# Kernel tuning notes

Hardware: AMD Instinct MI355X
Metric: run time of the kernel (lower is better)

## Reference

```python
import jax, jax.numpy as jnp
import numpy as np

D_IN, D_K, D_V = 512, 256, 256
B, S = 8, 2048

def _glorot(key, shape):
    fan_in, fan_out = shape[0], shape[-1]
    lim = np.sqrt(6.0 / (fan_in + fan_out))
    return jax.random.uniform(key, shape, jnp.float32, -lim, lim)

def setup_inputs() -> dict:
    key = jax.random.key(0)
    ks = jax.random.split(key, 9)
    return {
        "q_in": jax.random.normal(ks[0], (B, S, D_IN), jnp.float32),
        "k_in": jax.random.normal(ks[1], (B, S, D_IN), jnp.float32),
        "v_in": jax.random.normal(ks[2], (B, S, D_IN), jnp.float32),
        "Wq": _glorot(ks[3], (D_IN, D_K)),
        "bq": _glorot(ks[4], (1, D_K))[0],
        "Wk": _glorot(ks[5], (D_IN, D_K)),
        "bk": _glorot(ks[6], (1, D_K))[0],
        "Wv": _glorot(ks[7], (D_IN, D_V)),
        "bv": _glorot(ks[8], (1, D_V))[0],
    }

def reference(q_in, k_in, v_in, Wq, bq, Wk, bk, Wv, bv):
    # Dense projections (with bias, glorot-init'ed bias as in the original)
    q = q_in @ Wq + bq            # [B, S, d_k]
    k = k_in @ Wk + bk            # [B, S, d_k]
    v = v_in @ Wv + bv            # [B, S, d_v]
    scale = 1.0 / np.sqrt(D_K).astype(np.float32)
    # full attention matrix, scaled (map_fn in original == elementwise divide)
    attn = jnp.einsum('bqd,bkd->bqk', q, k) * scale  # [B, S, S]
    attn = jax.nn.softmax(attn, axis=-1)
    return jnp.einsum('bqk,bkd->bqd', attn, v)       # [B, S, d_v]
```

## Files before the change

### kernel.cpp

```cpp
#include <hip/hip_runtime.h>
#include <hip/hip_bf16.h>


typedef __attribute__((ext_vector_type(4))) float f32x4;
typedef __attribute__((ext_vector_type(8))) short s16x8;
typedef __attribute__((ext_vector_type(4))) short s16x4;
typedef unsigned int u32;

static __device__ __forceinline__ short f2bf(float x) {
  __hip_bfloat16 h = __float2bfloat16(x);
  return *reinterpret_cast<short*>(&h);
}
static __device__ __forceinline__ u32 pack2bf(float lo, float hi) {
  return (u32)(unsigned short)f2bf(lo) | ((u32)(unsigned short)f2bf(hi) << 16);
}
static __device__ __forceinline__ void gload16(const void* g, void* l) {
  __builtin_amdgcn_global_load_lds(
      (const __attribute__((address_space(1))) u32*)g,
      (__attribute__((address_space(3))) u32*)l, 16, 0, 0);
}

__global__ __launch_bounds__(256) void proj3(
    const float* __restrict__ q_in, const float* __restrict__ k_in,
    const float* __restrict__ v_in, const float* __restrict__ bq,
    const float* __restrict__ bk, const float* __restrict__ bv,
    const float* __restrict__ Wq, const float* __restrict__ Wk,
    const float* __restrict__ Wv, short* __restrict__ qs,
    char* __restrict__ ks, char* __restrict__ vt) {
  const int flat = blockIdx.x;
  const int ord = (flat & 7) * 96 + (flat >> 3);
  const int z = ord >> 8;
  const int rem = ord & 255;
  const int n0 = (rem & 1) * 128;
  const int m0 = (rem >> 1) * 128;
  const float* X = z == 0 ? q_in : z == 1 ? k_in : v_in;
  const float* W = z == 0 ? Wq : z == 1 ? Wk : Wv;
  const float* bias = z == 0 ? bq : z == 1 ? bk : bv;
  const float sc = z == 0 ? 0.0625f : 1.0f;

  __shared__ short As[128][40];
  __shared__ short Bs[128][40];

  const int tid = threadIdx.x;
  const int lane = tid & 63;
  const int wid = tid >> 6;
  const int wr = wid >> 1, wc = wid & 1;
  const int g = lane >> 4, c = lane & 15;

  f32x4 acc[4][4];
#pragma unroll
  for (int m = 0; m < 4; m++)
#pragma unroll
    for (int n = 0; n < 4; n++) acc[m][n] = (f32x4)0.0f;

  const int arow = tid >> 1, ahalf = tid & 1;
  const int bn = tid & 127, bhalf = tid >> 7;

  for (int kt = 0; kt < 16; ++kt) {
    const int k0 = kt * 32;
    const float* ap = &X[(m0 + arow) * 512 + k0 + ahalf * 16];
    f32x4 a0 = *(const f32x4*)(ap + 0);
    f32x4 a1 = *(const f32x4*)(ap + 4);
    f32x4 a2 = *(const f32x4*)(ap + 8);
    f32x4 a3 = *(const f32x4*)(ap + 12);
    float wv[16];
#pragma unroll
    for (int j = 0; j < 16; j++)
      wv[j] = W[(k0 + bhalf * 16 + j) * 256 + n0 + bn] * sc;
    __syncthreads();
    s16x8 ac0, ac1, w0, w1;
#pragma unroll
    for (int i = 0; i < 4; i++) {
      ac0[i] = f2bf(a0[i]);
      ac0[i + 4] = f2bf(a1[i]);
      ac1[i] = f2bf(a2[i]);
      ac1[i + 4] = f2bf(a3[i]);
    }
#pragma unroll
    for (int j = 0; j < 8; j++) {
      w0[j] = f2bf(wv[j]);
      w1[j] = f2bf(wv[8 + j]);
    }
    *(s16x8*)&As[arow][ahalf * 16 + 0] = ac0;
    *(s16x8*)&As[arow][ahalf * 16 + 8] = ac1;
    *(s16x8*)&Bs[bn][bhalf * 16 + 0] = w0;
    *(s16x8*)&Bs[bn][bhalf * 16 + 8] = w1;
    __syncthreads();
    s16x8 af[4], bfr[4];
#pragma unroll
    for (int m = 0; m < 4; m++)
      af[m] = *(const s16x8*)&As[wr * 64 + m * 16 + c][g * 8];
#pragma unroll
    for (int n = 0; n < 4; n++)
      bfr[n] = *(const s16x8*)&Bs[wc * 64 + n * 16 + c][g * 8];
#pragma unroll
    for (int m = 0; m < 4; m++)
#pragma unroll
      for (int n = 0; n < 4; n++)
        acc[m][n] = __builtin_amdgcn_mfma_f32_16x16x32_bf16(af[m], bfr[n],
                                                            acc[m][n], 0, 0, 0);
  }

  float bv4[4];
#pragma unroll
  for (int n = 0; n < 4; n++) bv4[n] = bias[n0 + wc * 64 + n * 16 + c] * sc;

  if (z == 0) {
#pragma unroll
    for (int m = 0; m < 4; m++) {
      const int row0 = m0 + wr * 64 + m * 16 + g * 4;
#pragma unroll
      for (int n = 0; n < 4; n++) {
        const int col = n0 + wc * 64 + n * 16 + c;
#pragma unroll
        for (int r = 0; r < 4; r++)
          qs[(row0 + r) * 512 + col] = f2bf(acc[m][n][r] + bv4[n]);
      }
    }
  } else if (z == 1) {
#pragma unroll
    for (int m = 0; m < 4; m++) {
      const int row0 = m0 + wr * 64 + m * 16 + g * 4;
#pragma unroll
      for (int n = 0; n < 4; n++) {
        const int col = n0 + wc * 64 + n * 16 + c;
#pragma unroll
        for (int r = 0; r < 4; r++) {
          const int rowg = row0 + r;
          const int bb = rowg >> 11, s = rowg & 2047;
          const int tt = s >> 5, rr = s & 31;
          const u32 off = (u32)(rr * 512 + col * 2) ^ ((u32)(rr & 7) << 4);
          *(short*)(ks + ((size_t)(bb * 64 + tt) << 14) + off) =
              f2bf(acc[m][n][r] + bv4[n]);
        }
      }
    }
  } else {
#pragma unroll
    for (int m = 0; m < 4; m++) {
      const int row0 = m0 + wr * 64 + m * 16 + g * 4;
      const int bb = row0 >> 11, s = row0 & 2047;
      const int tt = s >> 5, kvl = s & 31;
#pragma unroll
      for (int n = 0; n < 4; n++) {
        const int col = n0 + wc * 64 + n * 16 + c;
        s16x4 pk;
#pragma unroll
        for (int r = 0; r < 4; r++) pk[r] = f2bf(acc[m][n][r] + bv4[n]);
        const u32 off = (u32)(col * 64 + kvl * 2) ^ ((u32)(col & 7) << 4);
        *(s16x4*)(vt + ((size_t)(bb * 64 + tt) << 14) + off) = pk;
      }
    }
  }
}

__global__ __launch_bounds__(512, 1) void attn_fused(
    const short* __restrict__ qs, const char* __restrict__ ksb,
    const char* __restrict__ vtb, float* __restrict__ out) {
  const int bid = blockIdx.x;
  const int b = bid & 7;
  const int q0 = (bid >> 3) * 64;

  __shared__ __align__(16) char smem[141312];

  const int tid = threadIdx.x;
  const int lane = tid & 63;
  const int wid = tid >> 6;
  const int grp = wid >> 2;
  const int wq = wid & 3;
  const int gtid = tid & 255;
  const int g = lane >> 4, c = lane & 15;

  const char* ktiles = ksb + ((size_t)b << 20);
  const char* vtiles = vtb + ((size_t)b << 20);

  char* gbase = smem + grp * 65536;
  short* Ps = (short*)(smem + 131072 + wid * 1280);

  s16x8 qf[8];
  {
    const int qrow = (b << 11) + q0 + wq * 16 + c;
#pragma unroll
    for (int d = 0; d < 8; d++)
      qf[d] = *(const s16x8*)&qs[qrow * 512 + d * 32 + g * 8];
  }

  f32x4 o[16];
#pragma unroll
  for (int f = 0; f < 16; f++) o[f] = (f32x4)0.0f;
  float m_l = -1e30f;
  float l_l = 0.f;

  const u32 xr = (u32)(c & 7) << 4;

  auto STAGE = [&](int t, int sel) {
    const size_t toff = (size_t)(grp * 32 + t) << 14;
    char* kd = gbase + sel * 32768;
    char* vd = kd + 16384;
    const char* ksrc = ktiles + toff + gtid * 16;
    const char* vsrc = vtiles + toff + gtid * 16;
#pragma unroll
    for (int i = 0; i < 4; i++) {
      gload16(ksrc + i * 4096, kd + gtid * 16 + i * 4096);
      gload16(vsrc + i * 4096, vd + gtid * 16 + i * 4096);
    }
  };

  STAGE(0, 0);
  __syncthreads();

  for (int t = 0; t < 32; ++t) {
    const int sel = t & 1;
    if (t < 31) STAGE(t + 1, sel ^ 1);

    const char* Kb = gbase + sel * 32768;
    const char* Vb = Kb + 16384;

    f32x4 sf[2];
    sf[0] = (f32x4)0.0f;
    sf[1] = (f32x4)0.0f;
    __builtin_amdgcn_s_setprio(1);
#pragma unroll
    for (int d = 0; d < 8; ++d) {
      const u32 k0off = ((u32)(c * 512 + d * 64 + g * 16)) ^ xr;
      const s16x8 kf0 = *(const s16x8*)(Kb + k0off);
      const s16x8 kf1 = *(const s16x8*)(Kb + (k0off + 8192));
      sf[0] = __builtin_amdgcn_mfma_f32_16x16x32_bf16(kf0, qf[d], sf[0], 0, 0, 0);
      sf[1] = __builtin_amdgcn_mfma_f32_16x16x32_bf16(kf1, qf[d], sf[1], 0, 0, 0);
    }
    __builtin_amdgcn_s_setprio(0);

    float mx = sf[0][0];
#pragma unroll
    for (int nf = 0; nf < 2; nf++)
#pragma unroll
      for (int r = 0; r < 4; r++) mx = fmaxf(mx, sf[nf][r]);
    mx = fmaxf(mx, __shfl_xor(mx, 16, 64));
    mx = fmaxf(mx, __shfl_xor(mx, 32, 64));
    if (__any(mx > m_l + 8.f)) {
      const float mn = fmaxf(m_l, mx);
      const float scr = __expf(m_l - mn);
      m_l = mn;
      l_l *= scr;
      float so[4];
#pragma unroll
      for (int r = 0; r < 4; r++) so[r] = __shfl(scr, g * 4 + r, 64);
#pragma unroll
      for (int f = 0; f < 16; f++)
#pragma unroll
        for (int r = 0; r < 4; r++) o[f][r] *= so[r];
    }
    float sum = 0.f;
#pragma unroll
    for (int nf = 0; nf < 2; nf++)
#pragma unroll
      for (int r = 0; r < 4; r++) {
        const float p = __expf(sf[nf][r] - m_l);
        sf[nf][r] = p;
        sum += p;
      }
    sum += __shfl_xor(sum, 16, 64);
    sum += __shfl_xor(sum, 32, 64);
    l_l += sum;

#pragma unroll
    for (int nf = 0; nf < 2; nf++) {
      const int base = c * 40 + nf * 16 + g * 4;
      *(u32*)&Ps[base] = pack2bf(sf[nf][0], sf[nf][1]);
      *(u32*)&Ps[base + 2] = pack2bf(sf[nf][2], sf[nf][3]);
    }

    const s16x8 pa = *(const s16x8*)&Ps[c * 40 + g * 8];
    __builtin_amdgcn_s_setprio(1);
#pragma unroll
    for (int f = 0; f < 16; ++f) {
      const u32 voff = ((u32)((f * 16 + c) * 64 + g * 16)) ^ xr;
      const s16x8 vf = *(const s16x8*)(Vb + voff);
      o[f] = __builtin_amdgcn_mfma_f32_16x16x32_bf16(pa, vf, o[f], 0, 0, 0);
    }
    __builtin_amdgcn_s_setprio(0);

    __syncthreads();
  }

  float(*Om)[260] = (float(*)[260])smem;
  float(*Ml)[2] = (float(*)[2])(smem + 66560);
  float m0r[4], l0r[4];
#pragma unroll
  for (int r = 0; r < 4; r++) {
    m0r[r] = __shfl(m_l, g * 4 + r, 64);
    l0r[r] = __shfl(l_l, g * 4 + r, 64);
  }
  if (grp == 1) {
#pragma unroll
    for (int f = 0; f < 16; f++)
#pragma unroll
      for (int r = 0; r < 4; r++)
        Om[wq * 16 + g * 4 + r][f * 16 + c] = o[f][r];
    if (g == 0) {
      Ml[wq * 16 + c][0] = m_l;
      Ml[wq * 16 + c][1] = l_l;
    }
  }
  __syncthreads();
  if (grp == 0) {
    float e0v[4], e1v[4], inv[4];
#pragma unroll
    for (int r = 0; r < 4; r++) {
      const int rw = wq * 16 + g * 4 + r;
      const float m1 = Ml[rw][0], l1 = Ml[rw][1];
      const float ms = fmaxf(m0r[r], m1);
      e0v[r] = __expf(m0r[r] - ms);
      e1v[r] = __expf(m1 - ms);
      inv[r] = 1.0f / (l0r[r] * e0v[r] + l1 * e1v[r]);
    }
#pragma unroll
    for (int f = 0; f < 16; f++) {
#pragma unroll
      for (int r = 0; r < 4; r++) {
        const int rw = wq * 16 + g * 4 + r;
        out[((b << 11) + q0 + rw) * 256 + f * 16 + c] =
            (o[f][r] * e0v[r] + Om[rw][f * 16 + c] * e1v[r]) * inv[r];
      }
    }
  }
}

extern "C" void kernel_launch(void* const* d_in, const int* in_sizes, int n_in,
                              void* d_out, int out_size, void* d_ws,
                              size_t ws_size, hipStream_t stream) {
  const float* q_in = (const float*)d_in[0];
  const float* k_in = (const float*)d_in[1];
  const float* v_in = (const float*)d_in[2];
  const float* Wq = (const float*)d_in[3];
  const float* bq = (const float*)d_in[4];
  const float* Wk = (const float*)d_in[5];
  const float* bk = (const float*)d_in[6];
  const float* Wv = (const float*)d_in[7];
  const float* bv = (const float*)d_in[8];
  float* out = (float*)d_out;

  char* ws = (char*)d_ws;
  short* qsb = (short*)d_out;
  char* ksb = ws;
  char* vtb = ws + (8 << 20);

  proj3<<<dim3(768), dim3(256), 0, stream>>>(q_in, k_in, v_in, bq, bk, bv, Wq,
                                             Wk, Wv, qsb, ksb, vtb);
  attn_fused<<<dim3(256), dim3(512), 0, stream>>>(qsb, ksb, vtb, out);
}
```

Measured before the change: 105.0 us.

## Split attention KV range across four wave groups and retile projection GEMM

The attention kernel moves from 512 to 1024 threads, so four wave groups each handle a quarter of the KV sequence (16 tiles each). The per-group K/V staging is single-buffered with two barriers per iteration in place of double-buffered prefetch, and the four partial softmax states are merged through shared memory. The projection kernel switches to 64x256 tiles with full-width N, which re-reads each input row once instead of twice. The intent is to spread the serial KV loop over more waves; the cost is lost load/compute overlap and a serialized four-step reduction.

```diff
diff --git a/kernel.cpp b/kernel.cpp
--- a/kernel.cpp
+++ b/kernel.cpp
@@ -27,19 +27,16 @@
     const float* __restrict__ Wq, const float* __restrict__ Wk,
     const float* __restrict__ Wv, short* __restrict__ qs,
     char* __restrict__ ks, char* __restrict__ vt) {
-  const int flat = blockIdx.x;
-  const int ord = (flat & 7) * 96 + (flat >> 3);
-  const int z = ord >> 8;
-  const int rem = ord & 255;
-  const int n0 = (rem & 1) * 128;
-  const int m0 = (rem >> 1) * 128;
+  const int bid = blockIdx.x;
+  const int z = bid % 3;
+  const int m0 = (bid / 3) * 64;
   const float* X = z == 0 ? q_in : z == 1 ? k_in : v_in;
   const float* W = z == 0 ? Wq : z == 1 ? Wk : Wv;
   const float* bias = z == 0 ? bq : z == 1 ? bk : bv;
   const float sc = z == 0 ? 0.0625f : 1.0f;
 
-  __shared__ short As[128][40];
-  __shared__ short Bs[128][40];
+  __shared__ short As[64][40];
+  __shared__ short Bs[256][40];
 
   const int tid = threadIdx.x;
   const int lane = tid & 63;
@@ -47,83 +44,77 @@
   const int wr = wid >> 1, wc = wid & 1;
   const int g = lane >> 4, c = lane & 15;
 
-  f32x4 acc[4][4];
-#pragma unroll
-  for (int m = 0; m < 4; m++)
-#pragma unroll
-    for (int n = 0; n < 4; n++) acc[m][n] = (f32x4)0.0f;
-
-  const int arow = tid >> 1, ahalf = tid & 1;
-  const int bn = tid & 127, bhalf = tid >> 7;
+  f32x4 acc[2][8];
+#pragma unroll
+  for (int m = 0; m < 2; m++)
+#pragma unroll
+    for (int n = 0; n < 8; n++) acc[m][n] = (f32x4)0.0f;
+
+  const int arow = tid >> 2, aseg = tid & 3;
+  const int bn = tid;
 
   for (int kt = 0; kt < 16; ++kt) {
     const int k0 = kt * 32;
-    const float* ap = &X[(m0 + arow) * 512 + k0 + ahalf * 16];
+    const float* ap = &X[(m0 + arow) * 512 + k0 + aseg * 8];
     f32x4 a0 = *(const f32x4*)(ap + 0);
     f32x4 a1 = *(const f32x4*)(ap + 4);
-    f32x4 a2 = *(const f32x4*)(ap + 8);
-    f32x4 a3 = *(const f32x4*)(ap + 12);
-    float wv[16];
-#pragma unroll
-    for (int j = 0; j < 16; j++)
-      wv[j] = W[(k0 + bhalf * 16 + j) * 256 + n0 + bn] * sc;
-    __syncthreads();
-    s16x8 ac0, ac1, w0, w1;
+    float wv[32];
+#pragma unroll
+    for (int j = 0; j < 32; j++) wv[j] = W[(k0 + j) * 256 + bn] * sc;
+    __syncthreads();
+    s16x8 ac;
 #pragma unroll
     for (int i = 0; i < 4; i++) {
-      ac0[i] = f2bf(a0[i]);
-      ac0[i + 4] = f2bf(a1[i]);
-      ac1[i] = f2bf(a2[i]);
-      ac1[i + 4] = f2bf(a3[i]);
-    }
-#pragma unroll
-    for (int j = 0; j < 8; j++) {
-      w0[j] = f2bf(wv[j]);
-      w1[j] = f2bf(wv[8 + j]);
-    }
-    *(s16x8*)&As[arow][ahalf * 16 + 0] = ac0;
-    *(s16x8*)&As[arow][ahalf * 16 + 8] = ac1;
-    *(s16x8*)&Bs[bn][bhalf * 16 + 0] = w0;
-    *(s16x8*)&Bs[bn][bhalf * 16 + 8] = w1;
-    __syncthreads();
-    s16x8 af[4], bfr[4];
-#pragma unroll
-    for (int m = 0; m < 4; m++)
-      af[m] = *(const s16x8*)&As[wr * 64 + m * 16 + c][g * 8];
-#pragma unroll
-    for (int n = 0; n < 4; n++)
-      bfr[n] = *(const s16x8*)&Bs[wc * 64 + n * 16 + c][g * 8];
-#pragma unroll
-    for (int m = 0; m < 4; m++)
-#pragma unroll
-      for (int n = 0; n < 4; n++)
+      ac[i] = f2bf(a0[i]);
+      ac[i + 4] = f2bf(a1[i]);
+    }
+    *(s16x8*)&As[arow][aseg * 8] = ac;
+#pragma unroll
+    for (int s = 0; s < 4; s++) {
+      s16x8 w8;
+#pragma unroll
+      for (int j = 0; j < 8; j++) w8[j] = f2bf(wv[s * 8 + j]);
+      *(s16x8*)&Bs[bn][s * 8] = w8;
+    }
+    __syncthreads();
+    s16x8 af[2], bfr[8];
+#pragma unroll
+    for (int m = 0; m < 2; m++)
+      af[m] = *(const s16x8*)&As[wr * 32 + m * 16 + c][g * 8];
+#pragma unroll
+    for (int n = 0; n < 8; n++)
+      bfr[n] = *(const s16x8*)&Bs[wc * 128 + n * 16 + c][g * 8];
+#pragma unroll
+    for (int m = 0; m < 2; m++)
+#pragma unroll
+      for (int n = 0; n < 8; n++)
         acc[m][n] = __builtin_amdgcn_mfma_f32_16x16x32_bf16(af[m], bfr[n],
                                                             acc[m][n], 0, 0, 0);
   }
 
-  float bv4[4];
-#pragma unroll
-  for (int n = 0; n < 4; n++) bv4[n] = bias[n0 + wc * 64 + n * 16 + c] * sc;
+  float bv8[8];
+#pragma unroll
+  for (int n = 0; n < 8; n++) bv8[n] = bias[wc * 128 + n * 16 + c] * sc;
 
   if (z == 0) {
 #pragma unroll
-    for (int m = 0; m < 4; m++) {
-      const int row0 = m0 + wr * 64 + m * 16 + g * 4;
-#pragma unroll
-      for (int n = 0; n < 4; n++) {
-        const int col = n0 + wc * 64 + n * 16 + c;
+    for (int m = 0; m < 2; m++) {
+      const int row0 = m0 + wr * 32 + m * 16 + g * 4;
+#pragma unroll
+      for (int n = 0; n < 8; n++) {
+        const int col = wc * 128 + n * 16 + c;
 #pragma unroll
         for (int r = 0; r < 4; r++)
-          qs[(row0 + r) * 512 + col] = f2bf(acc[m][n][r] + bv4[n]);
+          qs[(row0 + r) * 512 + col] = f2bf(acc[m][n][r] + bv8[n]);
       }
     }
   } else if (z == 1) {
 #pragma unroll
-    for (int m = 0; m < 4; m++) {
-      const int row0 = m0 + wr * 64 + m * 16 + g * 4;
-#pragma unroll
-      for (int n = 0; n < 4; n++) {
-        const int col = n0 + wc * 64 + n * 16 + c;
+    for (int m = 0; m < 2; m++) {
+      const int row0 = m0 + wr * 32 + m * 16 + g * 4;
+#pragma unroll
+      for (int n = 0; n < 8; n++) {
+        const int col = wc * 128 + n * 16 + c;
 #pragma unroll
         for (int r = 0; r < 4; r++) {
           const int rowg = row0 + r;
@@ -131,22 +122,22 @@
           const int tt = s >> 5, rr = s & 31;
           const u32 off = (u32)(rr * 512 + col * 2) ^ ((u32)(rr & 7) << 4);
           *(short*)(ks + ((size_t)(bb * 64 + tt) << 14) + off) =
-              f2bf(acc[m][n][r] + bv4[n]);
+              f2bf(acc[m][n][r] + bv8[n]);
         }
       }
     }
   } else {
 #pragma unroll
-    for (int m = 0; m < 4; m++) {
-      const int row0 = m0 + wr * 64 + m * 16 + g * 4;
+    for (int m = 0; m < 2; m++) {
+      const int row0 = m0 + wr * 32 + m * 16 + g * 4;
       const int bb = row0 >> 11, s = row0 & 2047;
       const int tt = s >> 5, kvl = s & 31;
 #pragma unroll
-      for (int n = 0; n < 4; n++) {
-        const int col = n0 + wc * 64 + n * 16 + c;
+      for (int n = 0; n < 8; n++) {
+        const int col = wc * 128 + n * 16 + c;
         s16x4 pk;
 #pragma unroll
-        for (int r = 0; r < 4; r++) pk[r] = f2bf(acc[m][n][r] + bv4[n]);
+        for (int r = 0; r < 4; r++) pk[r] = f2bf(acc[m][n][r] + bv8[n]);
         const u32 off = (u32)(col * 64 + kvl * 2) ^ ((u32)(col & 7) << 4);
         *(s16x4*)(vt + ((size_t)(bb * 64 + tt) << 14) + off) = pk;
       }
@@ -154,14 +145,14 @@
   }
 }
 
-__global__ __launch_bounds__(512, 1) void attn_fused(
+__global__ __launch_bounds__(1024) void attn_fused(
     const short* __restrict__ qs, const char* __restrict__ ksb,
     const char* __restrict__ vtb, float* __restrict__ out) {
   const int bid = blockIdx.x;
   const int b = bid & 7;
   const int q0 = (bid >> 3) * 64;
 
-  __shared__ __align__(16) char smem[141312];
+  __shared__ __align__(16) char smem[153600];
 
   const int tid = threadIdx.x;
   const int lane = tid & 63;
@@ -174,8 +165,9 @@
   const char* ktiles = ksb + ((size_t)b << 20);
   const char* vtiles = vtb + ((size_t)b << 20);
 
-  char* gbase = smem + grp * 65536;
+  char* gbase = smem + grp * 32768;
   short* Ps = (short*)(smem + 131072 + wid * 1280);
+  float* Mlf = (float*)(smem + 151552);
 
   s16x8 qf[8];
   {
@@ -193,28 +185,25 @@
 
   const u32 xr = (u32)(c & 7) << 4;
 
-  auto STAGE = [&](int t, int sel) {
-    const size_t toff = (size_t)(grp * 32 + t) << 14;
-    char* kd = gbase + sel * 32768;
-    char* vd = kd + 16384;
+  auto STAGE = [&](int t) {
+    const size_t toff = (size_t)(grp * 16 + t) << 14;
     const char* ksrc = ktiles + toff + gtid * 16;
     const char* vsrc = vtiles + toff + gtid * 16;
+    char* kd = gbase + gtid * 16;
+    char* vd = gbase + 16384 + gtid * 16;
 #pragma unroll
     for (int i = 0; i < 4; i++) {
-      gload16(ksrc + i * 4096, kd + gtid * 16 + i * 4096);
-      gload16(vsrc + i * 4096, vd + gtid * 16 + i * 4096);
+      gload16(ksrc + i * 4096, kd + i * 4096);
+      gload16(vsrc + i * 4096, vd + i * 4096);
     }
   };
 
-  STAGE(0, 0);
+  STAGE(0);
   __syncthreads();
 
-  for (int t = 0; t < 32; ++t) {
-    const int sel = t & 1;
-    if (t < 31) STAGE(t + 1, sel ^ 1);
-
-    const char* Kb = gbase + sel * 32768;
-    const char* Vb = Kb + 16384;
+  for (int t = 0; t < 16; ++t) {
+    const char* Kb = gbase;
+    const char* Vb = gbase + 16384;
 
     f32x4 sf[2];
     sf[0] = (f32x4)0.0f;
@@ -281,48 +270,56 @@
     __builtin_amdgcn_s_setprio(0);
 
     __syncthreads();
-  }
-
-  float(*Om)[260] = (float(*)[260])smem;
-  float(*Ml)[2] = (float(*)[2])(smem + 66560);
-  float m0r[4], l0r[4];
+    if (t < 15) STAGE(t + 1);
+    __syncthreads();
+  }
+
+  if (g == 0) {
+    Mlf[(grp * 64 + wq * 16 + c) * 2 + 0] = m_l;
+    Mlf[(grp * 64 + wq * 16 + c) * 2 + 1] = l_l;
+  }
+  __syncthreads();
+  float eown[4], inv4[4];
 #pragma unroll
   for (int r = 0; r < 4; r++) {
-    m0r[r] = __shfl(m_l, g * 4 + r, 64);
-    l0r[r] = __shfl(l_l, g * 4 + r, 64);
-  }
-  if (grp == 1) {
+    const int rw = wq * 16 + g * 4 + r;
+    float ms = -1e30f;
+#pragma unroll
+    for (int gg = 0; gg < 4; gg++) ms = fmaxf(ms, Mlf[(gg * 64 + rw) * 2]);
+    float den = 0.f;
+#pragma unroll
+    for (int gg = 0; gg < 4; gg++)
+      den += __expf(Mlf[(gg * 64 + rw) * 2] - ms) * Mlf[(gg * 64 + rw) * 2 + 1];
+    eown[r] = __expf(Mlf[(grp * 64 + rw) * 2] - ms);
+    inv4[r] = 1.0f / den;
+  }
+  float* Omf = (float*)smem;
+  for (int gg = 0; gg < 4; ++gg) {
+    if (grp == gg) {
+#pragma unroll
+      for (int f = 0; f < 16; f++)
+#pragma unroll
+        for (int r = 0; r < 4; r++) {
+          const int rw = wq * 16 + g * 4 + r;
+          const int idx = rw * 260 + f * 16 + c;
+          const float v = eown[r] * o[f][r];
+          if (gg == 0)
+            Omf[idx] = v;
+          else
+            Omf[idx] += v;
+        }
+    }
+    __syncthreads();
+  }
+  if (grp == 0) {
 #pragma unroll
     for (int f = 0; f < 16; f++)
-#pragma unroll
-      for (int r = 0; r < 4; r++)
-        Om[wq * 16 + g * 4 + r][f * 16 + c] = o[f][r];
-    if (g == 0) {
-      Ml[wq * 16 + c][0] = m_l;
-      Ml[wq * 16 + c][1] = l_l;
-    }
-  }
-  __syncthreads();
-  if (grp == 0) {
-    float e0v[4], e1v[4], inv[4];
-#pragma unroll
-    for (int r = 0; r < 4; r++) {
-      const int rw = wq * 16 + g * 4 + r;
-      const float m1 = Ml[rw][0], l1 = Ml[rw][1];
-      const float ms = fmaxf(m0r[r], m1);
-      e0v[r] = __expf(m0r[r] - ms);
-      e1v[r] = __expf(m1 - ms);
-      inv[r] = 1.0f / (l0r[r] * e0v[r] + l1 * e1v[r]);
-    }
-#pragma unroll
-    for (int f = 0; f < 16; f++) {
 #pragma unroll
       for (int r = 0; r < 4; r++) {
         const int rw = wq * 16 + g * 4 + r;
         out[((b << 11) + q0 + rw) * 256 + f * 16 + c] =
-            (o[f][r] * e0v[r] + Om[rw][f * 16 + c] * e1v[r]) * inv[r];
-      }
-    }
+            Omf[rw * 260 + f * 16 + c] * inv4[r];
+      }
   }
 }
 
@@ -347,5 +344,5 @@
 
   proj3<<<dim3(768), dim3(256), 0, stream>>>(q_in, k_in, v_in, bq, bk, bv, Wq,
                                              Wk, Wv, qsb, ksb, vtb);
-  attn_fused<<<dim3(256), dim3(512), 0, stream>>>(qsb, ksb, vtb, out);
-}
+  attn_fused<<<dim3(256), dim3(1024), 0, stream>>>(qsb, ksb, vtb, out);
+}
```

New measurement: 161.0 us. 53.3% more time.
